# Kernel optimization log

Measured on AMD Instinct MI355X. Metric: run time of the kernel, lower is better.

## Reference

```python
import jax, jax.numpy as jnp
import numpy as np

EMB = 512
H = 8
DK = EMB // H          # 64
MAX_SEQ = 768
TOPK = MAX_SEQ // 2    # 384


def setup_inputs() -> dict:
    key = jax.random.key(0)
    ks = jax.random.split(key, 16)
    B, S, E = 1, MAX_SEQ, EMB

    def w(k, shape):
        return jax.random.normal(k, shape, dtype=jnp.float32) * 0.02

    return {
        "x": jax.random.normal(ks[0], (B, S, E), dtype=jnp.float32),
        # main attention projections (Linear weights stored as (in, out))
        "Wq": w(ks[1], (E, E)), "bq": w(ks[2], (E,)),
        "Wk": w(ks[3], (E, E)), "bk": w(ks[4], (E,)),
        "Wv": w(ks[5], (E, E)), "bv": w(ks[6], (E,)),
        "Wo": w(ks[7], (E, E)), "bo": w(ks[8], (E,)),
        # indexer projections: wq -> (E, H*DK)=(E,E), wk -> (E, DK), weights_proj -> (E, H)
        "iq_W": w(ks[9], (E, H * DK)), "iq_b": w(ks[10], (H * DK,)),
        "ik_W": w(ks[11], (E, DK)),    "ik_b": w(ks[12], (DK,)),
        "wp_W": w(ks[13], (E, H)),     "wp_b": w(ks[14], (H,)),
    }


def reference(x, Wq, bq, Wk, bk, Wv, bv, Wo, bo, iq_W, iq_b, ik_W, ik_b, wp_W, wp_b):
    B, S, E = x.shape
    scaling = 1.0 / np.sqrt(DK)

    def split_heads(z):  # (B,S,E) -> (B,H,S,DK)
        return z.reshape(B, S, H, DK).transpose(0, 2, 1, 3)

    Q = split_heads(x @ Wq + bq)
    K = split_heads(x @ Wk + bk)
    V = split_heads(x @ Wv + bv)

    # --- indexer: per-token relevance scores ---
    q_idx = (x @ iq_W + iq_b).reshape(B, S, H, DK).transpose(0, 2, 1, 3)  # (B,H,S,DK)
    k_idx = x @ ik_W + ik_b                                               # (B,S,DK)
    w_idx = x @ wp_W + wp_b                                               # (B,S,H)
    score = jax.nn.relu(jnp.einsum('bhsd,btd->bhst', q_idx, k_idx))       # (B,H,S,S)
    indexer_score = jnp.einsum('bhst,bsh->bst', score, w_idx)             # (B,S,S)

    # --- top-k selection (set-equivalent to argpartition in the original) ---
    topk_idx = jax.lax.top_k(indexer_score, TOPK)[1]                      # (B,S,TOPK) int32

    # --- gather sparse K/V per query token ---
    def gather_b(Zb, idxb):  # Zb:(H,S,DK), idxb:(S,TOPK) -> (H,S,TOPK,DK)
        return Zb[:, idxb, :]
    K_s = jax.vmap(gather_b)(K, topk_idx)  # (B,H,S,TOPK,DK)
    V_s = jax.vmap(gather_b)(V, topk_idx)  # (B,H,S,TOPK,DK)

    # --- sparse attention over selected tokens ---
    sc = jnp.einsum('bhsd,bhskd->bhsk', Q, K_s) * scaling  # (B,H,S,TOPK)
    wts = jax.nn.softmax(sc, axis=-1)
    attn = jnp.einsum('bhsk,bhskd->bhsd', wts, V_s)        # (B,H,S,DK)

    out = attn.transpose(0, 2, 1, 3).reshape(B, S, E) @ Wo + bo
    return out
```

## Files before the change

### kernel.cpp

```cpp
#include <hip/hip_runtime.h>
#include <hip/hip_bf16.h>
#include <math.h>

#define S 768
#define E 512
#define H 8
#define DK 64
#define TOPK 384

typedef short bf16x8 __attribute__((ext_vector_type(8)));
typedef float f32x4 __attribute__((ext_vector_type(4)));

__device__ __forceinline__ unsigned short f2bf(float x) {
  unsigned u = __float_as_uint(x);
  unsigned r = u + 0x7FFFu + ((u >> 16) & 1u);
  return (unsigned short)(r >> 16);
}
__device__ __forceinline__ float bf2f(unsigned short h) {
  return __uint_as_float(((unsigned)h) << 16);
}
__device__ __forceinline__ void split1(float x, unsigned short& h, unsigned short& l) {
  h = f2bf(x);
  l = f2bf(x - bf2f(h));
}
// ... 13 lines not shown
  return *reinterpret_cast<const bf16x8*>(p);
}

struct PrepTab {
  const float* src[8];
  unsigned short* hi[8];
  unsigned short* lo[8];
};

__global__ __launch_bounds__(256) void prep_kernel(PrepTab t) {
  const int seg = blockIdx.z;
  const int rows = (seg == 0) ? 768 : 512;
  const int cols = (seg == 5) ? 64 : ((seg == 6) ? 8 : 512);
  const int tx = (seg == 6) ? 2 : ((cols + 31) >> 5);
  const int ty = rows >> 5;
  if ((int)blockIdx.x >= tx || (int)blockIdx.y >= ty) return;
  const int r0 = blockIdx.y * 32, c0 = blockIdx.x * 32;
  const int tid = threadIdx.x;
  const int rl = tid >> 3, c4 = (tid & 7) << 2;
  const float* src = t.src[seg];
  if (seg == 0) {
    float4 v = *(const float4*)(src + (size_t)(r0 + rl) * cols + c0 + c4);
    unsigned short h[4], l[4];
    split1(v.x, h[0], l[0]); split1(v.y, h[1], l[1]);
    split1(v.z, h[2], l[2]); split1(v.w, h[3], l[3]);
    size_t off = (size_t)(r0 + rl) * cols + c0 + c4;
    *(ushort4*)(t.hi[seg] + off) = make_ushort4(h[0], h[1], h[2], h[3]);
    *(ushort4*)(t.lo[seg] + off) = make_ushort4(l[0], l[1], l[2], l[3]);
  } else {
    __shared__ float ts[32][33];
    #pragma unroll
    for (int j = 0; j < 4; ++j) {
      int c = c4 + j;
      ts[rl][c] = (c0 + c < cols) ? src[(size_t)(r0 + rl) * cols + c0 + c] : 0.0f;
    }
    __syncthreads();
    float v0 = ts[c4 + 0][rl], v1 = ts[c4 + 1][rl];
    float v2 = ts[c4 + 2][rl], v3 = ts[c4 + 3][rl];
    unsigned short h[4], l[4];
    split1(v0, h[0], l[0]); split1(v1, h[1], l[1]);
    split1(v2, h[2], l[2]); split1(v3, h[3], l[3]);
    size_t off = (size_t)(c0 + rl) * 512 + r0 + c4;
    *(ushort4*)(t.hi[seg] + off) = make_ushort4(h[0], h[1], h[2], h[3]);
    *(ushort4*)(t.lo[seg] + off) = make_ushort4(l[0], l[1], l[2], l[3]);
  }
}

struct ProjTab {
  const unsigned short* whi[6];
  const unsigned short* wlo[6];
  const float* bias[6];
};

__global__ __launch_bounds__(256) void proj_mfma_kernel(
    const unsigned short* __restrict__ Xhi, const unsigned short* __restrict__ Xlo,
    ProjTab pt,
    unsigned short* __restrict__ Qhi, unsigned short* __restrict__ Qlo,
    unsigned short* __restrict__ Khi, unsigned short* __restrict__ Klo,
    unsigned short* __restrict__ VThi,
    unsigned short* __restrict__ QIhi, unsigned short* __restrict__ QIlo,
    unsigned short* __restrict__ KIhi, unsigned short* __restrict__ KIlo,
    float* __restrict__ WI) {
  __shared__ __align__(16) unsigned short Ah[64][72];
  __shared__ __align__(16) unsigned short Al[64][72];
  __shared__ __align__(16) unsigned short Bh[64][72];
  __shared__ __align__(16) unsigned short Bl[64][72];
  const int bx = blockIdx.x;
  int seg, nt;
  if (bx < 32) { seg = bx >> 3; nt = bx & 7; }
  else         { seg = 4 + (bx - 32); nt = 0; }
  const int m0 = blockIdx.y * 64;
  const int n0 = nt * 64;
  const int tid = threadIdx.x;
  const int lane = tid & 63;
  const int wave = tid >> 6;
  const int mq = (wave >> 1) << 5;
  const int nq = (wave & 1) << 5;
  const int l15 = lane & 15;
  const int q8 = (lane >> 4) << 3;
  const int q4 = (lane >> 4) << 2;
  const unsigned short* Whi = pt.whi[seg];
  const unsigned short* Wlo = pt.wlo[seg];

  const int mm0 = tid >> 3,          kc0 = (tid & 7) << 3;
  const int mm1 = (tid + 256) >> 3,  kc1 = ((tid + 256) & 7) << 3;
  const size_t ga0 = (size_t)(m0 + mm0) * 512 + kc0;
  const size_t gb0 = (size_t)(n0 + mm0) * 512 + kc0;
  const size_t ga1 = (size_t)(m0 + mm1) * 512 + kc1;
  const size_t gb1 = (size_t)(n0 + mm1) * 512 + kc1;

  bf16x8 rah0 = ldfrag(Xhi + ga0), ral0 = ldfrag(Xlo + ga0);
  bf16x8 rbh0 = ldfrag(Whi + gb0), rbl0 = ldfrag(Wlo + gb0);
  bf16x8 rah1 = ldfrag(Xhi + ga1), ral1 = ldfrag(Xlo + ga1);
  bf16x8 rbh1 = ldfrag(Whi + gb1), rbl1 = ldfrag(Wlo + gb1);

  f32x4 acc[2][2] = {};
  for (int cc = 0; cc < 8; ++cc) {
    *(bf16x8*)&Ah[mm0][kc0] = rah0;
    *(bf16x8*)&Al[mm0][kc0] = ral0;
    *(bf16x8*)&Bh[mm0][kc0] = rbh0;
    *(bf16x8*)&Bl[mm0][kc0] = rbl0;
    *(bf16x8*)&Ah[mm1][kc1] = rah1;
    *(bf16x8*)&Al[mm1][kc1] = ral1;
    *(bf16x8*)&Bh[mm1][kc1] = rbh1;
    *(bf16x8*)&Bl[mm1][kc1] = rbl1;
    if (cc < 7) {
      const size_t o = (size_t)(cc + 1) << 6;
      rah0 = ldfrag(Xhi + ga0 + o); ral0 = ldfrag(Xlo + ga0 + o);
      rbh0 = ldfrag(Whi + gb0 + o); rbl0 = ldfrag(Wlo + gb0 + o);
      rah1 = ldfrag(Xhi + ga1 + o); ral1 = ldfrag(Xlo + ga1 + o);
      rbh1 = ldfrag(Whi + gb1 + o); rbl1 = ldfrag(Wlo + gb1 + o);
    }
    __syncthreads();
    #pragma unroll
    for (int ki = 0; ki < 64; ki += 32) {
      const int kk = ki + q8;
      bf16x8 ah0 = *(const bf16x8*)&Ah[mq + l15][kk];
      bf16x8 al0 = *(const bf16x8*)&Al[mq + l15][kk];
      bf16x8 ah1 = *(const bf16x8*)&Ah[mq + 16 + l15][kk];
      bf16x8 al1 = *(const bf16x8*)&Al[mq + 16 + l15][kk];
      bf16x8 bh0 = *(const bf16x8*)&Bh[nq + l15][kk];
      bf16x8 bl0 = *(const bf16x8*)&Bl[nq + l15][kk];
      bf16x8 bh1 = *(const bf16x8*)&Bh[nq + 16 + l15][kk];
      bf16x8 bl1 = *(const bf16x8*)&Bl[nq + 16 + l15][kk];
      mfma3(acc[0][0], ah0, al0, bh0, bl0);
      mfma3(acc[0][1], ah0, al0, bh1, bl1);
      mfma3(acc[1][0], ah1, al1, bh0, bl0);
      mfma3(acc[1][1], ah1, al1, bh1, bl1);
    }
    __syncthreads();
  }

  const float* bias = pt.bias[seg];
  #pragma unroll
  for (int ntt = 0; ntt < 2; ++ntt) {
    const int nloc = n0 + nq + ntt * 16 + l15;
    const float bv = (seg == 5 && nloc >= 8) ? 0.0f : bias[nloc];
    #pragma unroll
    for (int mt = 0; mt < 2; ++mt) {
      #pragma unroll
      for (int r = 0; r < 4; ++r) {
        const int m = m0 + mq + mt * 16 + q4 + r;
        const float v = acc[mt][ntt][r] + bv;
        unsigned short h16, l16;
        if (seg == 0) {
          split1(v, h16, l16);
          Qhi[(size_t)m * 512 + nloc] = h16;
          Qlo[(size_t)m * 512 + nloc] = l16;
        } else if (seg == 1) {
          const int hh = nloc >> 6, dd = nloc & 63;
          split1(v, h16, l16);
          Khi[((size_t)hh * S + m) * 64 + dd] = h16;
          Klo[((size_t)hh * S + m) * 64 + dd] = l16;
        } else if (seg == 2) {
          VThi[((size_t)(nloc >> 6) * 64 + (nloc & 63)) * S + m] = f2bf(v);
        } else if (seg == 3) {
          split1(v, h16, l16);
          QIhi[(size_t)m * 512 + nloc] = h16;
          QIlo[(size_t)m * 512 + nloc] = l16;
        } else if (seg == 4) {
          split1(v, h16, l16);
          KIhi[(size_t)m * 64 + nloc] = h16;
          KIlo[(size_t)m * 64 + nloc] = l16;
        } else {
          if (nloc < 8) WI[(size_t)m * 8 + nloc] = v;
        }
      }
    }
  }
}

__global__ __launch_bounds__(256) void indexer_mfma_kernel(
    const unsigned short* __restrict__ QIhi, const unsigned short* __restrict__ QIlo,
    const unsigned short* __restrict__ KIhi, const unsigned short* __restrict__ KIlo,
    const float* __restrict__ WI, float* __restrict__ ISC) {
  __shared__ __align__(16) unsigned short Qh[32][136];
  __shared__ __align__(16) unsigned short Ql[32][136];
  __shared__ float wis[32][8];
  const int s0 = blockIdx.y * 32, t0 = blockIdx.x * 64;
  const int tid = threadIdx.x;
  const int lane = tid & 63;
  const int wave = tid >> 6;
  const int mq = (wave >> 1) << 4;
  const int nqb = (wave & 1) << 5;
  const int l15 = lane & 15;
  const int q8 = (lane >> 4) << 3;
  const int q4 = (lane >> 4) << 2;
  wis[tid >> 3][tid & 7] = WI[(size_t)(s0 + (tid >> 3)) * 8 + (tid & 7)];

  const size_t brow0 = (size_t)(t0 + nqb + l15) * 64;
  const size_t brow1 = (size_t)(t0 + nqb + 16 + l15) * 64;
  bf16x8 kfh[2][2], kfl[2][2];
  #pragma unroll
  for (int kk = 0; kk < 2; ++kk) {
    const int kb = kk * 32 + q8;
    kfh[kk][0] = ldfrag(KIhi + brow0 + kb);
    kfl[kk][0] = ldfrag(KIlo + brow0 + kb);
    kfh[kk][1] = ldfrag(KIhi + brow1 + kb);
    kfl[kk][1] = ldfrag(KIlo + brow1 + kb);
  }

  const int smm = tid >> 3;
  const int skc = (tid & 7) << 4;
  const size_t qbase = (size_t)(s0 + smm) * 512 + skc;
  bf16x8 rq0 = ldfrag(QIhi + qbase);
  bf16x8 rq1 = ldfrag(QIhi + qbase + 8);
  bf16x8 rq2 = ldfrag(QIlo + qbase);
  bf16x8 rq3 = ldfrag(QIlo + qbase + 8);

  float accI[2][4] = {};
  for (int hp = 0; hp < 4; ++hp) {
    __syncthreads();
    *(bf16x8*)&Qh[smm][skc]     = rq0;
    *(bf16x8*)&Qh[smm][skc + 8] = rq1;
    *(bf16x8*)&Ql[smm][skc]     = rq2;
    *(bf16x8*)&Ql[smm][skc + 8] = rq3;
    if (hp < 3) {
      const size_t g = qbase + (size_t)(hp + 1) * 128;
      rq0 = ldfrag(QIhi + g);
      rq1 = ldfrag(QIhi + g + 8);
      rq2 = ldfrag(QIlo + g);
      rq3 = ldfrag(QIlo + g + 8);
    }
    __syncthreads();
    #pragma unroll
    for (int hh = 0; hh < 2; ++hh) {
      const int h = hp * 2 + hh;
      f32x4 d[2] = {};
      #pragma unroll
      for (int kk = 0; kk < 2; ++kk) {
        const int ka = hh * 64 + kk * 32 + q8;
        bf16x8 ah = *(const bf16x8*)&Qh[mq + l15][ka];
        bf16x8 al = *(const bf16x8*)&Ql[mq + l15][ka];
        mfma3(d[0], ah, al, kfh[kk][0], kfl[kk][0]);
        mfma3(d[1], ah, al, kfh[kk][1], kfl[kk][1]);
      }
      #pragma unroll
      for (int r = 0; r < 4; ++r) {
        const float w = wis[mq + q4 + r][h];
        accI[0][r] = fmaf(fmaxf(d[0][r], 0.0f), w, accI[0][r]);
        accI[1][r] = fmaf(fmaxf(d[1][r], 0.0f), w, accI[1][r]);
      }
    }
  }
  #pragma unroll
  for (int ntt = 0; ntt < 2; ++ntt)
    #pragma unroll
    for (int r = 0; r < 4; ++r)
      ISC[(size_t)(s0 + mq + q4 + r) * S + t0 + nqb + ntt * 16 + l15] = accI[ntt][r];
}

__global__ __launch_bounds__(256) void topk_kernel(
    const float* __restrict__ ISC, unsigned* __restrict__ Mask,
    float* __restrict__ Sum, float* __restrict__ ATTacc) {
  __shared__ unsigned ordv[768];
  __shared__ int hist[256];
  __shared__ int gsum[16];
  __shared__ int sc[256];
  __shared__ unsigned mw[24];
  __shared__ unsigned sh_prefix;
  __shared__ int sh_R;
  const int s = blockIdx.x;
  const int tid = threadIdx.x;
  for (int i = tid; i < 768; i += 256) {
    float f = ISC[s * 768 + i] + 0.0f;
    unsigned u = __float_as_uint(f);
    ordv[i] = (u & 0x80000000u) ? ~u : (u | 0x80000000u);
  }
  {
    const float4 z4 = {0.0f, 0.0f, 0.0f, 0.0f};
    if (tid < 128) *(float4*)(ATTacc + (size_t)s * 512 + tid * 4) = z4;
  }
  if (tid < 24) mw[tid] = 0u;
  if (tid < H) Sum[tid * S + s] = 0.0f;
  if (tid == 0) { sh_prefix = 0u; sh_R = TOPK; }
  __syncthreads();
  for (int pass = 0; pass < 4; ++pass) {
    const int shift = 24 - pass * 8;
    hist[tid] = 0;
    __syncthreads();
    const unsigned pm = (pass == 0) ? 0u : (0xFFFFFFFFu << (shift + 8));
    const unsigned pref = sh_prefix;
    for (int i = tid; i < 768; i += 256) {
      unsigned o = ordv[i];
      if ((o & pm) == pref) atomicAdd(&hist[(o >> shift) & 255], 1);
    }
    __syncthreads();
    if (tid < 16) {
      int t = 0;
      #pragma unroll
      for (int k = 0; k < 16; ++k) t += hist[tid * 16 + k];
      gsum[tid] = t;
    }
    __syncthreads();
    if (tid == 0) {
      int R = sh_R;
      int G = 0;
      int g = 15;
      for (; g > 0; --g) {
        if (G + gsum[g] >= R) break;
        G += gsum[g];
      }
      int b = 15;
      for (; b > 0; --b) {
        int c = hist[g * 16 + b];
        if (G + c >= R) break;
        G += c;
      }
      sh_prefix = sh_prefix | ((unsigned)(g * 16 + b) << shift);
      sh_R = R - G;
    }
    __syncthreads();
  }
  const unsigned thr = sh_prefix;
  const int need_eq = sh_R;
  const int base = tid * 3;
  unsigned o0 = ordv[base], o1 = ordv[base + 1], o2 = ordv[base + 2];
  int c = (o0 == thr) + (o1 == thr) + (o2 == thr);
  sc[tid] = c;
  __syncthreads();
  for (int off = 1; off < 256; off <<= 1) {
    int v = (tid >= off) ? sc[tid - off] : 0;
    __syncthreads();
    sc[tid] += v;
    __syncthreads();
  }
  int rank = sc[tid] - c;
  if (o0 > thr || (o0 == thr && rank < need_eq))
    atomicOr(&mw[base >> 5], 1u << (base & 31));
  if (o0 == thr) ++rank;
  if (o1 > thr || (o1 == thr && rank < need_eq))
    atomicOr(&mw[(base + 1) >> 5], 1u << ((base + 1) & 31));
  if (o1 == thr) ++rank;
  if (o2 > thr || (o2 == thr && rank < need_eq))
    atomicOr(&mw[(base + 2) >> 5], 1u << ((base + 2) & 31));
  __syncthreads();
  if (tid < 24) Mask[s * 24 + tid] = mw[tid];
}

__global__ __launch_bounds__(512) void sattn_kernel(
    const unsigned short* __restrict__ Qhi, const unsigned short* __restrict__ Qlo,
    const unsigned short* __restrict__ Khi, const unsigned short* __restrict__ Klo,
    const unsigned short* __restrict__ VThi,
    const unsigned* __restrict__ Mask, float* __restrict__ ATTacc,
    float* __restrict__ Sum) {
  __shared__ __align__(16) unsigned short Ksh[64][72];
  __shared__ __align__(16) unsigned short Ksl[64][72];
  __shared__ __align__(16) unsigned short Vsh[64][72];
  __shared__ __align__(16) unsigned short Pshi[64][72];
  __shared__ __align__(16) unsigned short Pslo[64][72];
  __shared__ unsigned msk[64][6];
  __shared__ float rsumf[64];
  const int ks = blockIdx.x;
  const int s0 = blockIdx.y * 64;
  const int h  = blockIdx.z;
  const int tid = threadIdx.x;
  const int lane = tid & 63;
  const int wave = tid >> 6;
  const int l15 = lane & 15;
  const int q8 = (lane >> 4) << 3;
  const int q4 = (lane >> 4) << 2;
  const int mq = (wave >> 1) << 4;
  const int nqq = (wave & 1) << 4;
  const int db = (wave & 1) << 5;

  if (tid < 384) msk[tid & 63][tid >> 6] =
      Mask[(size_t)(s0 + (tid & 63)) * 24 + ks * 6 + (tid >> 6)];
  if (tid < 64) rsumf[tid] = 0.0f;

  const size_t qrow = (size_t)(s0 + mq + l15) * 512 + h * 64;
  bf16x8 qh0 = ldfrag(Qhi + qrow + 0 + q8);
  bf16x8 ql0 = ldfrag(Qlo + qrow + 0 + q8);
  bf16x8 qh1 = ldfrag(Qhi + qrow + 32 + q8);
  bf16x8 ql1 = ldfrag(Qlo + qrow + 32 + q8);

  const int tr = tid >> 3;
  const int kc = (tid & 7) << 3;
  const size_t gkbase = ((size_t)h * S + ks * 192 + tr) * 64 + kc;
  const size_t gvbase = ((size_t)h * 64 + tr) * S + ks * 192 + kc;
  bf16x8 rkh = ldfrag(Khi + gkbase);
  bf16x8 rkl = ldfrag(Klo + gkbase);
  bf16x8 rv  = ldfrag(VThi + gvbase);

  f32x4 oacc[2] = {};
  for (int ct = 0; ct < 3; ++ct) {
    __syncthreads();
    *(bf16x8*)&Ksh[tr][kc] = rkh;
    *(bf16x8*)&Ksl[tr][kc] = rkl;
    *(bf16x8*)&Vsh[tr][kc] = rv;
    if (ct < 2) {
      rkh = ldfrag(Khi + gkbase + (size_t)(ct + 1) * 4096);
      rkl = ldfrag(Klo + gkbase + (size_t)(ct + 1) * 4096);
      rv  = ldfrag(VThi + gvbase + (size_t)(ct + 1) * 64);
    }
    __syncthreads();
    float esum[4] = {0.0f, 0.0f, 0.0f, 0.0f};
    #pragma unroll
    for (int cp = 0; cp < 2; ++cp) {
      const int tcol = nqq + cp * 32;
      f32x4 d = {0.0f, 0.0f, 0.0f, 0.0f};
      bf16x8 bh0 = *(const bf16x8*)&Ksh[tcol + l15][q8];
      bf16x8 bl0 = *(const bf16x8*)&Ksl[tcol + l15][q8];
      bf16x8 bh1 = *(const bf16x8*)&Ksh[tcol + l15][32 + q8];
      bf16x8 bl1 = *(const bf16x8*)&Ksl[tcol + l15][32 + q8];
      mfma3(d, qh0, ql0, bh0, bl0);
      mfma3(d, qh1, ql1, bh1, bl1);
      const int tl = ct * 64 + tcol + l15;
      #pragma unroll
      for (int r = 0; r < 4; ++r) {
        const int srow = mq + q4 + r;
        const unsigned w = msk[srow][tl >> 5];
        float e = ((w >> (tl & 31)) & 1u) ? __expf(d[r] * 0.125f) : 0.0f;
        unsigned short h16, l16;
        split1(e, h16, l16);
        Pshi[srow][tcol + l15] = h16;
        Pslo[srow][tcol + l15] = l16;
        esum[r] += e;
      }
    }
    float v0 = esum[0], v1 = esum[1], v2 = esum[2], v3 = esum[3];
    #pragma unroll
    for (int off = 1; off < 16; off <<= 1) {
      v0 += __shfl_xor(v0, off);
      v1 += __shfl_xor(v1, off);
      v2 += __shfl_xor(v2, off);
      v3 += __shfl_xor(v3, off);
    }
    if (l15 == 0) {
      atomicAdd(&rsumf[mq + q4 + 0], v0);
      atomicAdd(&rsumf[mq + q4 + 1], v1);
      atomicAdd(&rsumf[mq + q4 + 2], v2);
      atomicAdd(&rsumf[mq + q4 + 3], v3);
    }
    __syncthreads();
    #pragma unroll
    for (int kk = 0; kk < 64; kk += 32) {
      bf16x8 pah = *(const bf16x8*)&Pshi[mq + l15][kk + q8];
      bf16x8 pal = *(const bf16x8*)&Pslo[mq + l15][kk + q8];
      #pragma unroll
      for (int dt = 0; dt < 2; ++dt) {
        bf16x8 vbh = *(const bf16x8*)&Vsh[db + dt * 16 + l15][kk + q8];
        mfma2(oacc[dt], pah, pal, vbh);
      }
    }
  }
  #pragma unroll
  for (int dt = 0; dt < 2; ++dt) {
    const int dd = db + dt * 16 + l15;
    #pragma unroll
    for (int r = 0; r < 4; ++r) {
      const int s = s0 + mq + q4 + r;
      atomicAdd(&ATTacc[(size_t)s * E + h * DK + dd], oacc[dt][r]);
    }
  }
  __syncthreads();
  if (tid < 64) atomicAdd(&Sum[(size_t)h * S + s0 + tid], rsumf[tid]);
}

__global__ __launch_bounds__(512) void out_mfma_kernel(
    const float* __restrict__ ATTacc, const float* __restrict__ Sum,
    const unsigned short* __restrict__ WoThi,
    const float* __restrict__ bo, float* __restrict__ out) {
  __shared__ float AccL[16][65];
  __shared__ float ivs[16][8];
  __shared__ __align__(16) unsigned short Ahi[16][520];
  __shared__ __align__(16) unsigned short Alo[16][520];
  const int tid512 = threadIdx.x;
  const int wave8 = tid512 >> 6;
  const int z = wave8 >> 2;
  const int wave = wave8 & 3;
  const int lane = tid512 & 63;
  const int m0 = blockIdx.y * 16;
  const int n0 = blockIdx.x * 64 + wave * 16;
  const int l15 = lane & 15;
  const int q8 = (lane >> 4) << 3;
  const int q4 = (lane >> 4) << 2;
  if (tid512 < 128) {
    const int r = tid512 >> 3, hh = tid512 & 7;
    ivs[r][hh] = 1.0f / Sum[(size_t)hh * S + m0 + r];
  }
  __syncthreads();
  {
    const int row = tid512 >> 5;
    const int kb = (tid512 & 31) << 4;
    const float inv = ivs[row][kb >> 6];
    const float* src = ATTacc + (size_t)(m0 + row) * 512 + kb;
    float4 a0 = *(const float4*)(src);
    float4 a1 = *(const float4*)(src + 4);
    float4 a2 = *(const float4*)(src + 8);
    float4 a3 = *(const float4*)(src + 12);
    float v[16] = {a0.x, a0.y, a0.z, a0.w, a1.x, a1.y, a1.z, a1.w,
                   a2.x, a2.y, a2.z, a2.w, a3.x, a3.y, a3.z, a3.w};
    #pragma unroll
    for (int i = 0; i < 16; ++i) {
      unsigned short hh, ll;
      split1(v[i] * inv, hh, ll);
      Ahi[row][kb + i] = hh;
      Alo[row][kb + i] = ll;
    }
  }
  __syncthreads();
  const size_t brow = (size_t)(n0 + l15) * 512;
  f32x4 acc = {};
  #pragma unroll
  for (int it = 0; it < 8; ++it) {
    const int ko = (z << 8) + (it << 5) + q8;
    bf16x8 ah = *(const bf16x8*)&Ahi[l15][ko];
    bf16x8 al = *(const bf16x8*)&Alo[l15][ko];
    bf16x8 bh = ldfrag(WoThi + brow + ko);
    mfma2(acc, ah, al, bh);
  }
  if (z == 1) {
    #pragma unroll
    for (int r = 0; r < 4; ++r)
      AccL[q4 + r][wave * 16 + l15] = acc[r];
  }
  __syncthreads();
  if (z == 0) {
    const int n = n0 + l15;
    const float bv = bo[n];
    #pragma unroll
    for (int r = 0; r < 4; ++r)
      out[(size_t)(m0 + q4 + r) * 512 + n] =
          acc[r] + AccL[q4 + r][wave * 16 + l15] + bv;
  }
}

extern "C" void kernel_launch(void* const* d_in, const int* in_sizes, int n_in,
                              void* d_out, int out_size, void* d_ws, size_t ws_size,
                              hipStream_t stream) {
  const float* x    = (const float*)d_in[0];
  const float* Wq   = (const float*)d_in[1];
  const float* bq   = (const float*)d_in[2];
  const float* Wk   = (const float*)d_in[3];
  const float* bk   = (const float*)d_in[4];
  const float* Wv   = (const float*)d_in[5];
  const float* bv   = (const float*)d_in[6];
  const float* Wo   = (const float*)d_in[7];
  const float* bo   = (const float*)d_in[8];
  const float* iqW  = (const float*)d_in[9];
  const float* iqb  = (const float*)d_in[10];
  const float* ikW  = (const float*)d_in[11];
  const float* ikb  = (const float*)d_in[12];
  const float* wpW  = (const float*)d_in[13];
  const float* wpb  = (const float*)d_in[14];

  float* ws = (float*)d_ws;
  float* WI   = ws;
  float* ISC  = WI + S * H;
  unsigned* Mask = (unsigned*)(ISC + S * S);
  float* Sum  = (float*)(Mask + S * 24);
  float* ATTacc = Sum + H * S;
  unsigned short* u = (unsigned short*)(ATTacc + S * E);
  unsigned short* Xhi  = u;             u += S * E;
  unsigned short* Xlo  = u;             u += S * E;
  unsigned short* Qhi  = u;             u += S * E;
  unsigned short* Qlo  = u;             u += S * E;
  unsigned short* Khi  = u;             u += S * E;
  unsigned short* Klo  = u;             u += S * E;
  unsigned short* VThi = u;             u += S * E;
  unsigned short* QIhi = u;             u += S * E;
  unsigned short* QIlo = u;             u += S * E;
  unsigned short* KIhi = u;             u += S * DK;
  unsigned short* KIlo = u;             u += S * DK;
  unsigned short* WTq_hi = u;           u += E * E;
  unsigned short* WTk_hi = u;           u += E * E;
  unsigned short* WTv_hi = u;           u += E * E;
  unsigned short* WTiq_hi = u;          u += E * E;
  unsigned short* WTik_hi = u;          u += 64 * E;
  unsigned short* WTwp_hi = u;          u += 64 * E;
  unsigned short* WTo_hi = u;           u += E * E;
  unsigned short* WTq_lo = u;           u += E * E;
  unsigned short* WTk_lo = u;           u += E * E;
  unsigned short* WTv_lo = u;           u += E * E;
  unsigned short* WTiq_lo = u;          u += E * E;
  unsigned short* WTik_lo = u;          u += 64 * E;
  unsigned short* WTwp_lo = u;          u += 64 * E;
  unsigned short* WTo_lo = u;           u += E * E;

  PrepTab prep;
  prep.src[0] = x;    prep.hi[0] = Xhi;     prep.lo[0] = Xlo;
  prep.src[1] = Wq;   prep.hi[1] = WTq_hi;  prep.lo[1] = WTq_lo;
  prep.src[2] = Wk;   prep.hi[2] = WTk_hi;  prep.lo[2] = WTk_lo;
  prep.src[3] = Wv;   prep.hi[3] = WTv_hi;  prep.lo[3] = WTv_lo;
  prep.src[4] = iqW;  prep.hi[4] = WTiq_hi; prep.lo[4] = WTiq_lo;
  prep.src[5] = ikW;  prep.hi[5] = WTik_hi; prep.lo[5] = WTik_lo;
  prep.src[6] = wpW;  prep.hi[6] = WTwp_hi; prep.lo[6] = WTwp_lo;
  prep.src[7] = Wo;   prep.hi[7] = WTo_hi;  prep.lo[7] = WTo_lo;

  ProjTab pt;
  pt.whi[0] = WTq_hi;  pt.wlo[0] = WTq_lo;  pt.bias[0] = bq;
  pt.whi[1] = WTk_hi;  pt.wlo[1] = WTk_lo;  pt.bias[1] = bk;
  pt.whi[2] = WTv_hi;  pt.wlo[2] = WTv_lo;  pt.bias[2] = bv;
  pt.whi[3] = WTiq_hi; pt.wlo[3] = WTiq_lo; pt.bias[3] = iqb;
  pt.whi[4] = WTik_hi; pt.wlo[4] = WTik_lo; pt.bias[4] = ikb;
  pt.whi[5] = WTwp_hi; pt.wlo[5] = WTwp_lo; pt.bias[5] = wpb;

  prep_kernel<<<dim3(16, 24, 8), dim3(256), 0, stream>>>(prep);
  proj_mfma_kernel<<<dim3(34, S / 64), dim3(256), 0, stream>>>(
      Xhi, Xlo, pt, Qhi, Qlo, Khi, Klo, VThi, QIhi, QIlo, KIhi, KIlo, WI);
  indexer_mfma_kernel<<<dim3(S / 64, S / 32), dim3(256), 0, stream>>>(
      QIhi, QIlo, KIhi, KIlo, WI, ISC);
  topk_kernel<<<dim3(S), dim3(256), 0, stream>>>(ISC, Mask, Sum, ATTacc);
  sattn_kernel<<<dim3(4, S / 64, H), dim3(512), 0, stream>>>(
      Qhi, Qlo, Khi, Klo, VThi, Mask, ATTacc, Sum);
  out_mfma_kernel<<<dim3(8, 48), dim3(512), 0, stream>>>(
      ATTacc, Sum, WTo_hi, bo, (float*)d_out);
}
```

Before: 139.5 us.

## Restructure sparse attention to per-block full key sweep, drop global atomics

The sparse attention kernel now gives each block 16 query rows and a single head, and sweeps all 768 keys in six chunks. K and V fragments are prefetched from registers and the P tile is double-buffered, replacing the old 4-way split over keys that merged results with global atomics. The kernel normalizes its own output and writes bf16 hi/lo split activations, so the ATTacc and Sum zeroing in topk and the normalize/split step in the output kernel are removed. The topk prefix scan also switches from a shared-memory Hillis-Steele loop with many barriers to wave shuffles. In exchange there are fewer blocks with more serial work each, and the K fragments are loaded straight from global memory without LDS sharing.

New measurement: 146.6 us. 5.1% more time.

```diff
diff --git a/kernel.cpp b/kernel.cpp
--- a/kernel.cpp
+++ b/kernel.cpp
@@ -288,12 +288,11 @@
 }
 
 __global__ __launch_bounds__(256) void topk_kernel(
-    const float* __restrict__ ISC, unsigned* __restrict__ Mask,
-    float* __restrict__ Sum, float* __restrict__ ATTacc) {
+    const float* __restrict__ ISC, unsigned* __restrict__ Mask) {
   __shared__ unsigned ordv[768];
   __shared__ int hist[256];
   __shared__ int gsum[16];
-  __shared__ int sc[256];
+  __shared__ int wtot[4];
   __shared__ unsigned mw[24];
   __shared__ unsigned sh_prefix;
   __shared__ int sh_R;
@@ -304,12 +303,7 @@
     unsigned u = __float_as_uint(f);
     ordv[i] = (u & 0x80000000u) ? ~u : (u | 0x80000000u);
   }
-  {
-    const float4 z4 = {0.0f, 0.0f, 0.0f, 0.0f};
-    if (tid < 128) *(float4*)(ATTacc + (size_t)s * 512 + tid * 4) = z4;
-  }
   if (tid < 24) mw[tid] = 0u;
-  if (tid < H) Sum[tid * S + s] = 0.0f;
   if (tid == 0) { sh_prefix = 0u; sh_R = TOPK; }
   __syncthreads();
   for (int pass = 0; pass < 4; ++pass) {
@@ -354,15 +348,19 @@
   const int base = tid * 3;
   unsigned o0 = ordv[base], o1 = ordv[base + 1], o2 = ordv[base + 2];
   int c = (o0 == thr) + (o1 == thr) + (o2 == thr);
-  sc[tid] = c;
+  const int lane = tid & 63, wv = tid >> 6;
+  int sum = c;
+  #pragma unroll
+  for (int off = 1; off < 64; off <<= 1) {
+    int v = __shfl_up(sum, off);
+    if (lane >= off) sum += v;
+  }
+  if (lane == 63) wtot[wv] = sum;
   __syncthreads();
-  for (int off = 1; off < 256; off <<= 1) {
-    int v = (tid >= off) ? sc[tid - off] : 0;
-    __syncthreads();
-    sc[tid] += v;
-    __syncthreads();
-  }
-  int rank = sc[tid] - c;
+  int rank = sum - c;
+  if (wv > 0) rank += wtot[0];
+  if (wv > 1) rank += wtot[1];
+  if (wv > 2) rank += wtot[2];
   if (o0 > thr || (o0 == thr && rank < need_eq))
     atomicOr(&mw[base >> 5], 1u << (base & 31));
   if (o0 == thr) ++rank;
@@ -379,127 +377,130 @@
     const unsigned short* __restrict__ Qhi, const unsigned short* __restrict__ Qlo,
     const unsigned short* __restrict__ Khi, const unsigned short* __restrict__ Klo,
     const unsigned short* __restrict__ VThi,
-    const unsigned* __restrict__ Mask, float* __restrict__ ATTacc,
-    float* __restrict__ Sum) {
-  __shared__ __align__(16) unsigned short Ksh[64][72];
-  __shared__ __align__(16) unsigned short Ksl[64][72];
-  __shared__ __align__(16) unsigned short Vsh[64][72];
-  __shared__ __align__(16) unsigned short Pshi[64][72];
-  __shared__ __align__(16) unsigned short Pslo[64][72];
-  __shared__ unsigned msk[64][6];
-  __shared__ float rsumf[64];
-  const int ks = blockIdx.x;
-  const int s0 = blockIdx.y * 64;
-  const int h  = blockIdx.z;
+    const unsigned* __restrict__ Mask,
+    unsigned short* __restrict__ AOhi, unsigned short* __restrict__ AOlo) {
+  __shared__ __align__(16) unsigned short Pshi[2][16][136];
+  __shared__ __align__(16) unsigned short Pslo[2][16][136];
+  __shared__ unsigned msk[16][24];
+  __shared__ float rsumf[16];
+  __shared__ float OfL[16][65];
+  const int s0 = blockIdx.x * 16;
+  const int h  = blockIdx.y;
   const int tid = threadIdx.x;
   const int lane = tid & 63;
-  const int wave = tid >> 6;
+  const int wq = tid >> 6;
   const int l15 = lane & 15;
   const int q8 = (lane >> 4) << 3;
   const int q4 = (lane >> 4) << 2;
-  const int mq = (wave >> 1) << 4;
-  const int nqq = (wave & 1) << 4;
-  const int db = (wave & 1) << 5;
-
-  if (tid < 384) msk[tid & 63][tid >> 6] =
-      Mask[(size_t)(s0 + (tid & 63)) * 24 + ks * 6 + (tid >> 6)];
-  if (tid < 64) rsumf[tid] = 0.0f;
-
-  const size_t qrow = (size_t)(s0 + mq + l15) * 512 + h * 64;
-  bf16x8 qh0 = ldfrag(Qhi + qrow + 0 + q8);
-  bf16x8 ql0 = ldfrag(Qlo + qrow + 0 + q8);
-  bf16x8 qh1 = ldfrag(Qhi + qrow + 32 + q8);
-  bf16x8 ql1 = ldfrag(Qlo + qrow + 32 + q8);
-
-  const int tr = tid >> 3;
-  const int kc = (tid & 7) << 3;
-  const size_t gkbase = ((size_t)h * S + ks * 192 + tr) * 64 + kc;
-  const size_t gvbase = ((size_t)h * 64 + tr) * S + ks * 192 + kc;
-  bf16x8 rkh = ldfrag(Khi + gkbase);
-  bf16x8 rkl = ldfrag(Klo + gkbase);
-  bf16x8 rv  = ldfrag(VThi + gvbase);
-
-  f32x4 oacc[2] = {};
-  for (int ct = 0; ct < 3; ++ct) {
-    __syncthreads();
-    *(bf16x8*)&Ksh[tr][kc] = rkh;
-    *(bf16x8*)&Ksl[tr][kc] = rkl;
-    *(bf16x8*)&Vsh[tr][kc] = rv;
-    if (ct < 2) {
-      rkh = ldfrag(Khi + gkbase + (size_t)(ct + 1) * 4096);
-      rkl = ldfrag(Klo + gkbase + (size_t)(ct + 1) * 4096);
-      rv  = ldfrag(VThi + gvbase + (size_t)(ct + 1) * 64);
-    }
-    __syncthreads();
-    float esum[4] = {0.0f, 0.0f, 0.0f, 0.0f};
-    #pragma unroll
-    for (int cp = 0; cp < 2; ++cp) {
-      const int tcol = nqq + cp * 32;
-      f32x4 d = {0.0f, 0.0f, 0.0f, 0.0f};
-      bf16x8 bh0 = *(const bf16x8*)&Ksh[tcol + l15][q8];
-      bf16x8 bl0 = *(const bf16x8*)&Ksl[tcol + l15][q8];
-      bf16x8 bh1 = *(const bf16x8*)&Ksh[tcol + l15][32 + q8];
-      bf16x8 bl1 = *(const bf16x8*)&Ksl[tcol + l15][32 + q8];
-      mfma3(d, qh0, ql0, bh0, bl0);
-      mfma3(d, qh1, ql1, bh1, bl1);
-      const int tl = ct * 64 + tcol + l15;
-      #pragma unroll
-      for (int r = 0; r < 4; ++r) {
-        const int srow = mq + q4 + r;
-        const unsigned w = msk[srow][tl >> 5];
-        float e = ((w >> (tl & 31)) & 1u) ? __expf(d[r] * 0.125f) : 0.0f;
-        unsigned short h16, l16;
-        split1(e, h16, l16);
-        Pshi[srow][tcol + l15] = h16;
-        Pslo[srow][tcol + l15] = l16;
-        esum[r] += e;
-      }
-    }
-    float v0 = esum[0], v1 = esum[1], v2 = esum[2], v3 = esum[3];
-    #pragma unroll
-    for (int off = 1; off < 16; off <<= 1) {
-      v0 += __shfl_xor(v0, off);
-      v1 += __shfl_xor(v1, off);
-      v2 += __shfl_xor(v2, off);
-      v3 += __shfl_xor(v3, off);
-    }
-    if (l15 == 0) {
-      atomicAdd(&rsumf[mq + q4 + 0], v0);
-      atomicAdd(&rsumf[mq + q4 + 1], v1);
-      atomicAdd(&rsumf[mq + q4 + 2], v2);
-      atomicAdd(&rsumf[mq + q4 + 3], v3);
-    }
-    __syncthreads();
-    #pragma unroll
-    for (int kk = 0; kk < 64; kk += 32) {
-      bf16x8 pah = *(const bf16x8*)&Pshi[mq + l15][kk + q8];
-      bf16x8 pal = *(const bf16x8*)&Pslo[mq + l15][kk + q8];
-      #pragma unroll
-      for (int dt = 0; dt < 2; ++dt) {
-        bf16x8 vbh = *(const bf16x8*)&Vsh[db + dt * 16 + l15][kk + q8];
-        mfma2(oacc[dt], pah, pal, vbh);
-      }
+  const int dq = wq & 3;
+  const int th = (wq >> 2) << 6;
+
+  if (tid < 384) {
+    const int r = tid / 24, w = tid - r * 24;
+    msk[r][w] = Mask[(size_t)(s0 + r) * 24 + w];
+  }
+  if (tid < 16) rsumf[tid] = 0.0f;
+
+  const size_t qrow = (size_t)(s0 + l15) * 512 + h * 64;
+  const bf16x8 qh0 = ldfrag(Qhi + qrow + q8);
+  const bf16x8 ql0 = ldfrag(Qlo + qrow + q8);
+  const bf16x8 qh1 = ldfrag(Qhi + qrow + 32 + q8);
+  const bf16x8 ql1 = ldfrag(Qlo + qrow + 32 + q8);
+
+  const size_t kbase = ((size_t)h * S + wq * 16 + l15) * 64;
+  const size_t vbase = ((size_t)h * 64 + dq * 16 + l15) * S + th + q8;
+
+  bf16x8 kh0 = ldfrag(Khi + kbase + q8);
+  bf16x8 kl0 = ldfrag(Klo + kbase + q8);
+  bf16x8 kh1 = ldfrag(Khi + kbase + 32 + q8);
+  bf16x8 kl1 = ldfrag(Klo + kbase + 32 + q8);
+  bf16x8 vb0 = ldfrag(VThi + vbase);
+  bf16x8 vb1 = ldfrag(VThi + vbase + 32);
+
+  f32x4 oacc = {};
+  float esum[4] = {0.0f, 0.0f, 0.0f, 0.0f};
+  const int colc = wq * 16 + l15;
+  __syncthreads();
+
+  for (int ct = 0; ct < 6; ++ct) {
+    const int cur = ct & 1;
+    f32x4 d = {};
+    mfma3(d, qh0, ql0, kh0, kl0);
+    mfma3(d, qh1, ql1, kh1, kl1);
+    bf16x8 nkh0, nkl0, nkh1, nkl1, nvb0, nvb1;
+    if (ct < 5) {
+      const size_t ko = kbase + (size_t)(ct + 1) * 8192;
+      nkh0 = ldfrag(Khi + ko + q8);
+      nkl0 = ldfrag(Klo + ko + q8);
+      nkh1 = ldfrag(Khi + ko + 32 + q8);
+      nkl1 = ldfrag(Klo + ko + 32 + q8);
+      const size_t vo = vbase + (size_t)(ct + 1) * 128;
+      nvb0 = ldfrag(VThi + vo);
+      nvb1 = ldfrag(VThi + vo + 32);
+    }
+    const int tl = ct * 128 + colc;
+    const unsigned wsh = tl & 31;
+    const int wrd = tl >> 5;
+    #pragma unroll
+    for (int r = 0; r < 4; ++r) {
+      const int srow = q4 + r;
+      const unsigned w = msk[srow][wrd];
+      float e = ((w >> wsh) & 1u) ? __expf(d[r] * 0.125f) : 0.0f;
+      unsigned short h16, l16;
+      split1(e, h16, l16);
+      Pshi[cur][srow][colc] = h16;
+      Pslo[cur][srow][colc] = l16;
+      esum[r] += e;
+    }
+    __syncthreads();
+    bf16x8 pah0 = *(const bf16x8*)&Pshi[cur][l15][th + q8];
+    bf16x8 pal0 = *(const bf16x8*)&Pslo[cur][l15][th + q8];
+    bf16x8 pah1 = *(const bf16x8*)&Pshi[cur][l15][th + 32 + q8];
+    bf16x8 pal1 = *(const bf16x8*)&Pslo[cur][l15][th + 32 + q8];
+    mfma2(oacc, pah0, pal0, vb0);
+    mfma2(oacc, pah1, pal1, vb1);
+    if (ct < 5) {
+      kh0 = nkh0; kl0 = nkl0; kh1 = nkh1; kl1 = nkl1;
+      vb0 = nvb0; vb1 = nvb1;
     }
   }
   #pragma unroll
-  for (int dt = 0; dt < 2; ++dt) {
-    const int dd = db + dt * 16 + l15;
+  for (int off = 1; off < 16; off <<= 1) {
+    esum[0] += __shfl_xor(esum[0], off);
+    esum[1] += __shfl_xor(esum[1], off);
+    esum[2] += __shfl_xor(esum[2], off);
+    esum[3] += __shfl_xor(esum[3], off);
+  }
+  if (l15 == 0) {
+    atomicAdd(&rsumf[q4 + 0], esum[0]);
+    atomicAdd(&rsumf[q4 + 1], esum[1]);
+    atomicAdd(&rsumf[q4 + 2], esum[2]);
+    atomicAdd(&rsumf[q4 + 3], esum[3]);
+  }
+  if (wq >= 4) {
+    #pragma unroll
+    for (int r = 0; r < 4; ++r) OfL[q4 + r][dq * 16 + l15] = oacc[r];
+  }
+  __syncthreads();
+  if (wq < 4) {
     #pragma unroll
     for (int r = 0; r < 4; ++r) {
-      const int s = s0 + mq + q4 + r;
-      atomicAdd(&ATTacc[(size_t)s * E + h * DK + dd], oacc[dt][r]);
-    }
-  }
-  __syncthreads();
-  if (tid < 64) atomicAdd(&Sum[(size_t)h * S + s0 + tid], rsumf[tid]);
+      const float o = oacc[r] + OfL[q4 + r][dq * 16 + l15];
+      const float inv = 1.0f / rsumf[q4 + r];
+      unsigned short h16, l16;
+      split1(o * inv, h16, l16);
+      const size_t a = (size_t)(s0 + q4 + r) * 512 + h * 64 + dq * 16 + l15;
+      AOhi[a] = h16;
+      AOlo[a] = l16;
+    }
+  }
 }
 
 __global__ __launch_bounds__(512) void out_mfma_kernel(
-    const float* __restrict__ ATTacc, const float* __restrict__ Sum,
+    const unsigned short* __restrict__ AhiG, const unsigned short* __restrict__ AloG,
     const unsigned short* __restrict__ WoThi,
     const float* __restrict__ bo, float* __restrict__ out) {
   __shared__ float AccL[16][65];
-  __shared__ float ivs[16][8];
   __shared__ __align__(16) unsigned short Ahi[16][520];
   __shared__ __align__(16) unsigned short Alo[16][520];
   const int tid512 = threadIdx.x;
@@ -512,29 +513,14 @@
   const int l15 = lane & 15;
   const int q8 = (lane >> 4) << 3;
   const int q4 = (lane >> 4) << 2;
-  if (tid512 < 128) {
-    const int r = tid512 >> 3, hh = tid512 & 7;
-    ivs[r][hh] = 1.0f / Sum[(size_t)hh * S + m0 + r];
-  }
-  __syncthreads();
   {
     const int row = tid512 >> 5;
-    const int kb = (tid512 & 31) << 4;
-    const float inv = ivs[row][kb >> 6];
-    const float* src = ATTacc + (size_t)(m0 + row) * 512 + kb;
-    float4 a0 = *(const float4*)(src);
-    float4 a1 = *(const float4*)(src + 4);
-    float4 a2 = *(const float4*)(src + 8);
-    float4 a3 = *(const float4*)(src + 12);
-    float v[16] = {a0.x, a0.y, a0.z, a0.w, a1.x, a1.y, a1.z, a1.w,
-                   a2.x, a2.y, a2.z, a2.w, a3.x, a3.y, a3.z, a3.w};
-    #pragma unroll
-    for (int i = 0; i < 16; ++i) {
-      unsigned short hh, ll;
-      split1(v[i] * inv, hh, ll);
-      Ahi[row][kb + i] = hh;
-      Alo[row][kb + i] = ll;
-    }
+    const int col = (tid512 & 31) << 4;
+    const size_t g = (size_t)(m0 + row) * 512 + col;
+    *(bf16x8*)&Ahi[row][col]     = ldfrag(AhiG + g);
+    *(bf16x8*)&Ahi[row][col + 8] = ldfrag(AhiG + g + 8);
+    *(bf16x8*)&Alo[row][col]     = ldfrag(AloG + g);
+    *(bf16x8*)&Alo[row][col + 8] = ldfrag(AloG + g + 8);
   }
   __syncthreads();
   const size_t brow = (size_t)(n0 + l15) * 512;
@@ -586,9 +572,7 @@
   float* WI   = ws;
   float* ISC  = WI + S * H;
   unsigned* Mask = (unsigned*)(ISC + S * S);
-  float* Sum  = (float*)(Mask + S * 24);
-  float* ATTacc = Sum + H * S;
-  unsigned short* u = (unsigned short*)(ATTacc + S * E);
+  unsigned short* u = (unsigned short*)(Mask + S * 24);
   unsigned short* Xhi  = u;             u += S * E;
   unsigned short* Xlo  = u;             u += S * E;
   unsigned short* Qhi  = u;             u += S * E;
@@ -600,6 +584,8 @@
   unsigned short* QIlo = u;             u += S * E;
   unsigned short* KIhi = u;             u += S * DK;
   unsigned short* KIlo = u;             u += S * DK;
+  unsigned short* AOhi = u;             u += S * E;
+  unsigned short* AOlo = u;             u += S * E;
   unsigned short* WTq_hi = u;           u += E * E;
   unsigned short* WTk_hi = u;           u += E * E;
   unsigned short* WTv_hi = u;           u += E * E;
@@ -638,9 +624,9 @@
       Xhi, Xlo, pt, Qhi, Qlo, Khi, Klo, VThi, QIhi, QIlo, KIhi, KIlo, WI);
   indexer_mfma_kernel<<<dim3(S / 64, S / 32), dim3(256), 0, stream>>>(
       QIhi, QIlo, KIhi, KIlo, WI, ISC);
-  topk_kernel<<<dim3(S), dim3(256), 0, stream>>>(ISC, Mask, Sum, ATTacc);
-  sattn_kernel<<<dim3(4, S / 64, H), dim3(512), 0, stream>>>(
-      Qhi, Qlo, Khi, Klo, VThi, Mask, ATTacc, Sum);
+  topk_kernel<<<dim3(S), dim3(256), 0, stream>>>(ISC, Mask);
+  sattn_kernel<<<dim3(S / 16, H), dim3(512), 0, stream>>>(
+      Qhi, Qlo, Khi, Klo, VThi, Mask, AOhi, AOlo);
   out_mfma_kernel<<<dim3(8, 48), dim3(512), 0, stream>>>(
-      ATTacc, Sum, WTo_hi, bo, (float*)d_out);
-}
+      AOhi, AOlo, WTo_hi, bo, (float*)d_out);
+}
```

## Overlap Q/K/V projections with indexer scoring; use wave-shuffle scan in top-k

Applied to the files above, without the earlier changes.

The projection kernel is split in two. Indexer projections (iq, ik, wp) go into a first small launch. The main Q/K/V projection blocks then share one launch with the indexer-score blocks, which depend only on the indexer projections. This lets the Q/K/V GEMMs run concurrently with indexer scoring instead of serially. Separately, the 256-element prefix scan in top-k changes from a shared-memory Hillis-Steele loop with many barriers to intra-wave shuffles plus a 4-entry cross-wave sum.

Result: slower. 144.0 us (+3.2%).

```diff
diff --git a/kernel.cpp b/kernel.cpp
--- a/kernel.cpp
+++ b/kernel.cpp
@@ -89,24 +89,19 @@
   const float* bias[6];
 };
 
-__global__ __launch_bounds__(256) void proj_mfma_kernel(
+struct ProjOut {
+  unsigned short *Qhi, *Qlo, *Khi, *Klo, *VThi, *QIhi, *QIlo, *KIhi, *KIlo;
+  float* WI;
+};
+
+__device__ __forceinline__ void proj_dev(
+    unsigned short* sm, int seg, int nt, int m0,
     const unsigned short* __restrict__ Xhi, const unsigned short* __restrict__ Xlo,
-    ProjTab pt,
-    unsigned short* __restrict__ Qhi, unsigned short* __restrict__ Qlo,
-    unsigned short* __restrict__ Khi, unsigned short* __restrict__ Klo,
-    unsigned short* __restrict__ VThi,
-    unsigned short* __restrict__ QIhi, unsigned short* __restrict__ QIlo,
-    unsigned short* __restrict__ KIhi, unsigned short* __restrict__ KIlo,
-    float* __restrict__ WI) {
-  __shared__ __align__(16) unsigned short Ah[64][72];
-  __shared__ __align__(16) unsigned short Al[64][72];
-  __shared__ __align__(16) unsigned short Bh[64][72];
-  __shared__ __align__(16) unsigned short Bl[64][72];
-  const int bx = blockIdx.x;
-  int seg, nt;
-  if (bx < 32) { seg = bx >> 3; nt = bx & 7; }
-  else         { seg = 4 + (bx - 32); nt = 0; }
-  const int m0 = blockIdx.y * 64;
+    const ProjTab& pt, const ProjOut& po) {
+  unsigned short (*Ah)[72] = (unsigned short(*)[72])(sm);
+  unsigned short (*Al)[72] = (unsigned short(*)[72])(sm + 4608);
+  unsigned short (*Bh)[72] = (unsigned short(*)[72])(sm + 9216);
+  unsigned short (*Bl)[72] = (unsigned short(*)[72])(sm + 13824);
   const int n0 = nt * 64;
   const int tid = threadIdx.x;
   const int lane = tid & 63;
@@ -182,39 +177,49 @@
         unsigned short h16, l16;
         if (seg == 0) {
           split1(v, h16, l16);
-          Qhi[(size_t)m * 512 + nloc] = h16;
-          Qlo[(size_t)m * 512 + nloc] = l16;
+          po.Qhi[(size_t)m * 512 + nloc] = h16;
+          po.Qlo[(size_t)m * 512 + nloc] = l16;
         } else if (seg == 1) {
           const int hh = nloc >> 6, dd = nloc & 63;
           split1(v, h16, l16);
-          Khi[((size_t)hh * S + m) * 64 + dd] = h16;
-          Klo[((size_t)hh * S + m) * 64 + dd] = l16;
+          po.Khi[((size_t)hh * S + m) * 64 + dd] = h16;
+          po.Klo[((size_t)hh * S + m) * 64 + dd] = l16;
         } else if (seg == 2) {
-          VThi[((size_t)(nloc >> 6) * 64 + (nloc & 63)) * S + m] = f2bf(v);
+          po.VThi[((size_t)(nloc >> 6) * 64 + (nloc & 63)) * S + m] = f2bf(v);
         } else if (seg == 3) {
           split1(v, h16, l16);
-          QIhi[(size_t)m * 512 + nloc] = h16;
-          QIlo[(size_t)m * 512 + nloc] = l16;
+          po.QIhi[(size_t)m * 512 + nloc] = h16;
+          po.QIlo[(size_t)m * 512 + nloc] = l16;
         } else if (seg == 4) {
           split1(v, h16, l16);
-          KIhi[(size_t)m * 64 + nloc] = h16;
-          KIlo[(size_t)m * 64 + nloc] = l16;
+          po.KIhi[(size_t)m * 64 + nloc] = h16;
+          po.KIlo[(size_t)m * 64 + nloc] = l16;
         } else {
-          if (nloc < 8) WI[(size_t)m * 8 + nloc] = v;
+          if (nloc < 8) po.WI[(size_t)m * 8 + nloc] = v;
         }
       }
     }
   }
 }
 
-__global__ __launch_bounds__(256) void indexer_mfma_kernel(
+__global__ __launch_bounds__(256) void proj_idx_kernel(
+    const unsigned short* __restrict__ Xhi, const unsigned short* __restrict__ Xlo,
+    ProjTab pt, ProjOut po) {
+  __shared__ __align__(16) unsigned short sm[18432];
+  const int bx = blockIdx.x + 24;
+  int seg, nt;
+  if (bx < 32) { seg = bx >> 3; nt = bx & 7; }
+  else         { seg = 4 + (bx - 32); nt = 0; }
+  proj_dev(sm, seg, nt, blockIdx.y * 64, Xhi, Xlo, pt, po);
+}
+
+__device__ __forceinline__ void indexer_dev(
+    unsigned short* sm, float (*wis)[8], int t0, int s0,
     const unsigned short* __restrict__ QIhi, const unsigned short* __restrict__ QIlo,
     const unsigned short* __restrict__ KIhi, const unsigned short* __restrict__ KIlo,
     const float* __restrict__ WI, float* __restrict__ ISC) {
-  __shared__ __align__(16) unsigned short Qh[32][136];
-  __shared__ __align__(16) unsigned short Ql[32][136];
-  __shared__ float wis[32][8];
-  const int s0 = blockIdx.y * 32, t0 = blockIdx.x * 64;
+  unsigned short (*Qh)[136] = (unsigned short(*)[136])(sm);
+  unsigned short (*Ql)[136] = (unsigned short(*)[136])(sm + 4352);
   const int tid = threadIdx.x;
   const int lane = tid & 63;
   const int wave = tid >> 6;
@@ -287,13 +292,32 @@
       ISC[(size_t)(s0 + mq + q4 + r) * S + t0 + nqb + ntt * 16 + l15] = accI[ntt][r];
 }
 
+__global__ __launch_bounds__(256) void fused_pq_idx_kernel(
+    const unsigned short* __restrict__ Xhi, const unsigned short* __restrict__ Xlo,
+    ProjTab pt, ProjOut po,
+    const unsigned short* __restrict__ QIhi, const unsigned short* __restrict__ QIlo,
+    const unsigned short* __restrict__ KIhi, const unsigned short* __restrict__ KIlo,
+    const float* __restrict__ WI, float* __restrict__ ISC) {
+  __shared__ __align__(16) unsigned short sm[18432];
+  __shared__ float wis[32][8];
+  const int bx = blockIdx.x;
+  if (bx < 24) {
+    proj_dev(sm, bx >> 3, bx & 7, blockIdx.y * 64, Xhi, Xlo, pt, po);
+  } else {
+    const int xi = bx - 24;
+    const int t0 = (xi >> 1) * 64;
+    const int s0 = ((xi & 1) * 12 + blockIdx.y) * 32;
+    indexer_dev(sm, wis, t0, s0, QIhi, QIlo, KIhi, KIlo, WI, ISC);
+  }
+}
+
 __global__ __launch_bounds__(256) void topk_kernel(
     const float* __restrict__ ISC, unsigned* __restrict__ Mask,
     float* __restrict__ Sum, float* __restrict__ ATTacc) {
   __shared__ unsigned ordv[768];
   __shared__ int hist[256];
   __shared__ int gsum[16];
-  __shared__ int sc[256];
+  __shared__ int wtot[4];
   __shared__ unsigned mw[24];
   __shared__ unsigned sh_prefix;
   __shared__ int sh_R;
@@ -354,15 +378,19 @@
   const int base = tid * 3;
   unsigned o0 = ordv[base], o1 = ordv[base + 1], o2 = ordv[base + 2];
   int c = (o0 == thr) + (o1 == thr) + (o2 == thr);
-  sc[tid] = c;
+  const int lane = tid & 63, wv = tid >> 6;
+  int sum = c;
+  #pragma unroll
+  for (int off = 1; off < 64; off <<= 1) {
+    int v = __shfl_up(sum, off);
+    if (lane >= off) sum += v;
+  }
+  if (lane == 63) wtot[wv] = sum;
   __syncthreads();
-  for (int off = 1; off < 256; off <<= 1) {
-    int v = (tid >= off) ? sc[tid - off] : 0;
-    __syncthreads();
-    sc[tid] += v;
-    __syncthreads();
-  }
-  int rank = sc[tid] - c;
+  int rank = sum - c;
+  if (wv > 0) rank += wtot[0];
+  if (wv > 1) rank += wtot[1];
+  if (wv > 2) rank += wtot[2];
   if (o0 > thr || (o0 == thr && rank < need_eq))
     atomicOr(&mw[base >> 5], 1u << (base & 31));
   if (o0 == thr) ++rank;
@@ -633,11 +661,18 @@
   pt.whi[4] = WTik_hi; pt.wlo[4] = WTik_lo; pt.bias[4] = ikb;
   pt.whi[5] = WTwp_hi; pt.wlo[5] = WTwp_lo; pt.bias[5] = wpb;
 
+  ProjOut po;
+  po.Qhi = Qhi;   po.Qlo = Qlo;
+  po.Khi = Khi;   po.Klo = Klo;
+  po.VThi = VThi;
+  po.QIhi = QIhi; po.QIlo = QIlo;
+  po.KIhi = KIhi; po.KIlo = KIlo;
+  po.WI = WI;
+
   prep_kernel<<<dim3(16, 24, 8), dim3(256), 0, stream>>>(prep);
-  proj_mfma_kernel<<<dim3(34, S / 64), dim3(256), 0, stream>>>(
-      Xhi, Xlo, pt, Qhi, Qlo, Khi, Klo, VThi, QIhi, QIlo, KIhi, KIlo, WI);
-  indexer_mfma_kernel<<<dim3(S / 64, S / 32), dim3(256), 0, stream>>>(
-      QIhi, QIlo, KIhi, KIlo, WI, ISC);
+  proj_idx_kernel<<<dim3(10, 12), dim3(256), 0, stream>>>(Xhi, Xlo, pt, po);
+  fused_pq_idx_kernel<<<dim3(48, 12), dim3(256), 0, stream>>>(
+      Xhi, Xlo, pt, po, QIhi, QIlo, KIhi, KIlo, WI, ISC);
   topk_kernel<<<dim3(S), dim3(256), 0, stream>>>(ISC, Mask, Sum, ATTacc);
   sattn_kernel<<<dim3(4, S / 64, H), dim3(512), 0, stream>>>(
       Qhi, Qlo, Khi, Klo, VThi, Mask, ATTacc, Sum);
```

## Use wave-shuffle prefix scan in topk, register V fragments and defer PV in sattn

Applied to the files above, without the earlier changes.

The topk kernel's shared-memory Hillis-Steele scan, with two barriers per step, is replaced by a per-wave __shfl_up scan plus a small cross-wave total, which removes many block barriers. In the sparse attention kernel, V fragments are loaded straight from global memory into registers instead of staged through shared memory. The P·V MFMA for each chunk is deferred to the start of the next iteration, so one barrier per chunk is dropped and it overlaps with the K staging. Row-sum reduction and its atomics move out of the loop to a single pass at the end, at the cost of more live registers and uncoalesced-style V fragment loads.

Measured after the change: 138.1 us. No clear change (-1.0%).

```diff
diff --git a/kernel.cpp b/kernel.cpp
--- a/kernel.cpp
+++ b/kernel.cpp
@@ -293,7 +293,7 @@
   __shared__ unsigned ordv[768];
   __shared__ int hist[256];
   __shared__ int gsum[16];
-  __shared__ int sc[256];
+  __shared__ int wtot[4];
   __shared__ unsigned mw[24];
   __shared__ unsigned sh_prefix;
   __shared__ int sh_R;
@@ -354,15 +354,19 @@
   const int base = tid * 3;
   unsigned o0 = ordv[base], o1 = ordv[base + 1], o2 = ordv[base + 2];
   int c = (o0 == thr) + (o1 == thr) + (o2 == thr);
-  sc[tid] = c;
-  __syncthreads();
-  for (int off = 1; off < 256; off <<= 1) {
-    int v = (tid >= off) ? sc[tid - off] : 0;
-    __syncthreads();
-    sc[tid] += v;
-    __syncthreads();
-  }
-  int rank = sc[tid] - c;
+  const int lane = tid & 63, wv = tid >> 6;
+  int sum = c;
+  #pragma unroll
+  for (int off = 1; off < 64; off <<= 1) {
+    int v = __shfl_up(sum, off);
+    if (lane >= off) sum += v;
+  }
+  if (lane == 63) wtot[wv] = sum;
+  __syncthreads();
+  int rank = sum - c;
+  if (wv > 0) rank += wtot[0];
+  if (wv > 1) rank += wtot[1];
+  if (wv > 2) rank += wtot[2];
   if (o0 > thr || (o0 == thr && rank < need_eq))
     atomicOr(&mw[base >> 5], 1u << (base & 31));
   if (o0 == thr) ++rank;
@@ -383,7 +387,6 @@
     float* __restrict__ Sum) {
   __shared__ __align__(16) unsigned short Ksh[64][72];
   __shared__ __align__(16) unsigned short Ksl[64][72];
-  __shared__ __align__(16) unsigned short Vsh[64][72];
   __shared__ __align__(16) unsigned short Pshi[64][72];
   __shared__ __align__(16) unsigned short Pslo[64][72];
   __shared__ unsigned msk[64][6];
@@ -406,32 +409,48 @@
   if (tid < 64) rsumf[tid] = 0.0f;
 
   const size_t qrow = (size_t)(s0 + mq + l15) * 512 + h * 64;
-  bf16x8 qh0 = ldfrag(Qhi + qrow + 0 + q8);
-  bf16x8 ql0 = ldfrag(Qlo + qrow + 0 + q8);
+  bf16x8 qh0 = ldfrag(Qhi + qrow + q8);
+  bf16x8 ql0 = ldfrag(Qlo + qrow + q8);
   bf16x8 qh1 = ldfrag(Qhi + qrow + 32 + q8);
   bf16x8 ql1 = ldfrag(Qlo + qrow + 32 + q8);
 
   const int tr = tid >> 3;
   const int kc = (tid & 7) << 3;
   const size_t gkbase = ((size_t)h * S + ks * 192 + tr) * 64 + kc;
-  const size_t gvbase = ((size_t)h * 64 + tr) * S + ks * 192 + kc;
   bf16x8 rkh = ldfrag(Khi + gkbase);
   bf16x8 rkl = ldfrag(Klo + gkbase);
-  bf16x8 rv  = ldfrag(VThi + gvbase);
-
+
+  const size_t vb0 = ((size_t)h * 64 + db + l15) * S + ks * 192 + q8;
+  bf16x8 v00 = ldfrag(VThi + vb0);
+  bf16x8 v01 = ldfrag(VThi + vb0 + 32);
+  bf16x8 v10 = ldfrag(VThi + vb0 + (size_t)16 * S);
+  bf16x8 v11 = ldfrag(VThi + vb0 + (size_t)16 * S + 32);
+
+  float esum[4] = {0.0f, 0.0f, 0.0f, 0.0f};
   f32x4 oacc[2] = {};
   for (int ct = 0; ct < 3; ++ct) {
     __syncthreads();
+    if (ct > 0) {
+      #pragma unroll
+      for (int kk = 0; kk < 64; kk += 32) {
+        bf16x8 pah = *(const bf16x8*)&Pshi[mq + l15][kk + q8];
+        bf16x8 pal = *(const bf16x8*)&Pslo[mq + l15][kk + q8];
+        mfma2(oacc[0], pah, pal, (kk == 0) ? v00 : v01);
+        mfma2(oacc[1], pah, pal, (kk == 0) ? v10 : v11);
+      }
+      const size_t vo = vb0 + (size_t)ct * 64;
+      v00 = ldfrag(VThi + vo);
+      v01 = ldfrag(VThi + vo + 32);
+      v10 = ldfrag(VThi + vo + (size_t)16 * S);
+      v11 = ldfrag(VThi + vo + (size_t)16 * S + 32);
+    }
     *(bf16x8*)&Ksh[tr][kc] = rkh;
     *(bf16x8*)&Ksl[tr][kc] = rkl;
-    *(bf16x8*)&Vsh[tr][kc] = rv;
     if (ct < 2) {
       rkh = ldfrag(Khi + gkbase + (size_t)(ct + 1) * 4096);
       rkl = ldfrag(Klo + gkbase + (size_t)(ct + 1) * 4096);
-      rv  = ldfrag(VThi + gvbase + (size_t)(ct + 1) * 64);
-    }
-    __syncthreads();
-    float esum[4] = {0.0f, 0.0f, 0.0f, 0.0f};
+    }
+    __syncthreads();
     #pragma unroll
     for (int cp = 0; cp < 2; ++cp) {
       const int tcol = nqq + cp * 32;
@@ -455,31 +474,14 @@
         esum[r] += e;
       }
     }
-    float v0 = esum[0], v1 = esum[1], v2 = esum[2], v3 = esum[3];
-    #pragma unroll
-    for (int off = 1; off < 16; off <<= 1) {
-      v0 += __shfl_xor(v0, off);
-      v1 += __shfl_xor(v1, off);
-      v2 += __shfl_xor(v2, off);
-      v3 += __shfl_xor(v3, off);
-    }
-    if (l15 == 0) {
-      atomicAdd(&rsumf[mq + q4 + 0], v0);
-      atomicAdd(&rsumf[mq + q4 + 1], v1);
-      atomicAdd(&rsumf[mq + q4 + 2], v2);
-      atomicAdd(&rsumf[mq + q4 + 3], v3);
-    }
-    __syncthreads();
-    #pragma unroll
-    for (int kk = 0; kk < 64; kk += 32) {
-      bf16x8 pah = *(const bf16x8*)&Pshi[mq + l15][kk + q8];
-      bf16x8 pal = *(const bf16x8*)&Pslo[mq + l15][kk + q8];
-      #pragma unroll
-      for (int dt = 0; dt < 2; ++dt) {
-        bf16x8 vbh = *(const bf16x8*)&Vsh[db + dt * 16 + l15][kk + q8];
-        mfma2(oacc[dt], pah, pal, vbh);
-      }
-    }
+  }
+  __syncthreads();
+  #pragma unroll
+  for (int kk = 0; kk < 64; kk += 32) {
+    bf16x8 pah = *(const bf16x8*)&Pshi[mq + l15][kk + q8];
+    bf16x8 pal = *(const bf16x8*)&Pslo[mq + l15][kk + q8];
+    mfma2(oacc[0], pah, pal, (kk == 0) ? v00 : v01);
+    mfma2(oacc[1], pah, pal, (kk == 0) ? v10 : v11);
   }
   #pragma unroll
   for (int dt = 0; dt < 2; ++dt) {
@@ -489,6 +491,19 @@
       const int s = s0 + mq + q4 + r;
       atomicAdd(&ATTacc[(size_t)s * E + h * DK + dd], oacc[dt][r]);
     }
+  }
+  #pragma unroll
+  for (int off = 1; off < 16; off <<= 1) {
+    esum[0] += __shfl_xor(esum[0], off);
+    esum[1] += __shfl_xor(esum[1], off);
+    esum[2] += __shfl_xor(esum[2], off);
+    esum[3] += __shfl_xor(esum[3], off);
+  }
+  if (l15 == 0) {
+    atomicAdd(&rsumf[q4 + 0 + mq], esum[0]);
+    atomicAdd(&rsumf[q4 + 1 + mq], esum[1]);
+    atomicAdd(&rsumf[q4 + 2 + mq], esum[2]);
+    atomicAdd(&rsumf[q4 + 3 + mq], esum[3]);
   }
   __syncthreads();
   if (tid < 64) atomicAdd(&Sum[(size_t)h * S + s0 + tid], rsumf[tid]);
```
